# Kernel optimization log

Measured on AMD Instinct MI355X. Metric: run time of the kernel, lower is better.

Reference implementation:

```python
import jax, jax.numpy as jnp
import numpy as np

D_MODEL = 1024
N_HEADS = 16
HEAD_DIM = D_MODEL // N_HEADS  # 64
WINDOW = 128
LOCAL_BLOCK = 256
LATENT_TOKENS = 64
LATENT_D = 256
LATENT_HEADS = 4
LATENT_HD = LATENT_D // LATENT_HEADS  # 64
NEG = -1e9


def setup_inputs() -> dict:
    key = jax.random.key(0)
    ks = jax.random.split(key, 14)
    B, S = 2, 4096
    s = 0.02
    f32 = jnp.float32
    return {
        "x": jax.random.normal(ks[0], (B, S, D_MODEL), f32),
        "qkv_w": jax.random.normal(ks[1], (D_MODEL, 3 * D_MODEL), f32) * s,
        "qkv_b": jnp.zeros((3 * D_MODEL,), f32),
        "rq_w": jax.random.normal(ks[2], (D_MODEL, LATENT_D), f32) * s,
        "rq_b": jnp.zeros((LATENT_D,), f32),
        "rkv_w": jax.random.normal(ks[3], (D_MODEL, 2 * LATENT_D), f32) * s,
        "rkv_b": jnp.zeros((2 * LATENT_D,), f32),
        "rout_w": jax.random.normal(ks[4], (LATENT_D, D_MODEL), f32) * s,
        "rout_b": jnp.zeros((D_MODEL,), f32),
        "out_w": jax.random.normal(ks[5], (D_MODEL, D_MODEL), f32) * s,
        "out_b": jnp.zeros((D_MODEL,), f32),
        "gl_w": jax.random.normal(ks[6], (HEAD_DIM, 1), f32) * s,
        "gr_w": jax.random.normal(ks[7], (HEAD_DIM, 1), f32) * s,
    }


def _local_attention(q, k, v):
    # q,k,v: [B,H,S,hd]. Blockwise causal local attention: query i attends to
    # keys at distance d with 0 < d <= WINDOW (strictly past, self excluded).
    B, H, S, hd = q.shape
    bs = min(S, max(WINDOW, LOCAL_BLOCK))
    nb = S // bs  # S chosen divisible by bs
    w = WINDOW
    L = bs + w - 1  # key span per query block
    k_pad = jnp.pad(k, ((0, 0), (0, 0), (w - 1, 0), (0, 0)))
    v_pad = jnp.pad(v, ((0, 0), (0, 0), (w - 1, 0), (0, 0)))
    starts = jnp.arange(nb) * bs
    idx = starts[:, None] + jnp.arange(L)[None, :]  # [nb,L] into padded axis
    kb = k_pad[:, :, idx]  # [B,H,nb,L,hd]
    vb = v_pad[:, :, idx]
    qb = q.reshape(B, H, nb, bs, hd)
    q_pos = starts[:, None] + jnp.arange(bs)[None, :]            # [nb,bs]
    k_gpos = starts[:, None] + jnp.arange(L)[None, :] - (w - 1)   # [nb,L]
    dist = q_pos[:, :, None] - k_gpos[:, None, :]                 # [nb,bs,L]
    allowed = (dist > 0) & (dist <= w) & (k_gpos[:, None, :] >= 0)
    scale = 1.0 / np.sqrt(hd)
    scores = jnp.einsum('bhnqd,bhnkd->bhnqk', qb, kb) * scale
    scores = jnp.where(allowed, scores, NEG)
    attn = jax.nn.softmax(scores, axis=-1)
    # query 0 has no valid keys (self excluded) -> output 0 for that row
    attn = jnp.where(allowed.any(-1)[None, None, :, :, None], attn, 0.0)
    out = jnp.einsum('bhnqk,bhnkd->bhnqd', attn, vb)
    return out.reshape(B, H, S, hd)


def reference(x, qkv_w, qkv_b, rq_w, rq_b, rkv_w, rkv_b, rout_w, rout_b,
              out_w, out_b, gl_w, gr_w):
    B, S, D = x.shape
    # ---- local branch ----
    qkv = x @ qkv_w + qkv_b  # [B,S,3D]
    q, k, v = jnp.split(qkv, 3, axis=-1)
    def heads(t):
        return t.reshape(B, S, N_HEADS, HEAD_DIM).transpose(0, 2, 1, 3)
    local = _local_attention(heads(q), heads(k), heads(v))  # [B,H,S,hd]
    # ---- pooled latents ----
    chunk = -(-S // min(LATENT_TOKENS, S))  # ceil; S divisible here
    nlat = S // chunk
    pooled = x.reshape(B, nlat, chunk, D).mean(axis=2)  # [B,L,D]
    chunk_ids = jnp.arange(S) // chunk                   # [S]
    # ---- latent cross-attention ----
    rq = (x @ rq_w + rq_b).reshape(B, S, LATENT_HEADS, LATENT_HD).transpose(0, 2, 1, 3)
    rkv = pooled @ rkv_w + rkv_b
    rk, rv = jnp.split(rkv, 2, axis=-1)
    rk = rk.reshape(B, nlat, LATENT_HEADS, LATENT_HD).transpose(0, 2, 1, 3)
    rv = rv.reshape(B, nlat, LATENT_HEADS, LATENT_HD).transpose(0, 2, 1, 3)
    lscale = 1.0 / np.sqrt(LATENT_HD)
    lscores = jnp.einsum('bhsd,bhld->bhsl', rq, rk) * lscale  # [B,Hl,S,L]
    lat_allowed = jnp.arange(nlat)[None, :] < chunk_ids[:, None]  # strictly past chunks
    lscores = jnp.where(lat_allowed[None, None], lscores, NEG)
    lattn = jax.nn.softmax(lscores, axis=-1)
    lattn = jnp.where(lat_allowed.any(-1)[None, None, :, None], lattn, 0.0)
    lat_out = jnp.einsum('bhsl,bhld->bhsd', lattn, rv)  # [B,Hl,S,hdl]
    lat_out = lat_out.transpose(0, 2, 1, 3).reshape(B, S, LATENT_D)
    remote = (lat_out @ rout_w + rout_b)                 # [B,S,D]
    remote_h = remote.reshape(B, S, N_HEADS, HEAD_DIM).transpose(0, 2, 1, 3)
    # ---- learned per-head gate mixing local/remote ----
    gate = jax.nn.sigmoid(local @ gl_w + remote_h @ gr_w)  # [B,H,S,1]
    mixed = gate * local + (1.0 - gate) * remote_h
    mixed = mixed.transpose(0, 2, 1, 3).reshape(B, S, D)
    return mixed @ out_w + out_b
```

## Files before the change

kernel.cpp:

```cpp
#include <hip/hip_runtime.h>

typedef __bf16 bf16;
typedef bf16 bf16x4 __attribute__((ext_vector_type(4)));
typedef bf16 bf16x8 __attribute__((ext_vector_type(8)));
typedef float f32x4 __attribute__((ext_vector_type(4)));

#define B_ 2
#define S_ 4096
#define D_ 1024
#define QSTR 3328

__device__ __forceinline__ void gload_lds16(const void* g, void* l) {
  __builtin_amdgcn_global_load_lds((const __attribute__((address_space(1))) void*)g,
                                   (__attribute__((address_space(3))) void*)l, 16, 0, 0);
}

__device__ __forceinline__ void transpose_block(
    const float* __restrict__ in, bf16* __restrict__ out, int K, int N,
    int bx, int by, float (*tile)[33], int tx, int ty)
{
  const int nb = bx * 32, kb = by * 32;
#pragma unroll
  for (int j = 0; j < 4; j++)
    tile[ty + j * 8][tx] = in[(size_t)(kb + ty + j * 8) * N + nb + tx];
  __syncthreads();
#pragma unroll
  for (int j = 0; j < 4; j++)
    out[(size_t)(nb + ty + j * 8) * K + kb + tx] = (bf16)tile[tx][ty + j * 8];
}

__global__ __launch_bounds__(256) void prep_kernel(
    const float* __restrict__ qkv_w, const float* __restrict__ rq_w,
    const float* __restrict__ rkv_w, const float* __restrict__ rout_w,
    const float* __restrict__ out_w, const float* __restrict__ x,
    const float* __restrict__ qkv_b, const float* __restrict__ rq_b,
    bf16* __restrict__ qkvr_wt, bf16* __restrict__ rkv_wt,
    bf16* __restrict__ rout_wt, bf16* __restrict__ out_wt,
    bf16* __restrict__ xb, float* __restrict__ qkvr_b)
{
  __shared__ float tile[32][33];
  const int t = threadIdx.x;
  const int tx = t & 31, ty = t >> 5;
  int bid = blockIdx.x;
  if (bid < 3072) {
    transpose_block(qkv_w, qkvr_wt, 1024, 3072, bid % 96, bid / 96, tile, tx, ty);
    return;
  }
  bid -= 3072;
  if (bid < 256) {
    transpose_block(rq_w, qkvr_wt + (size_t)3072 * 1024, 1024, 256, bid % 8, bid / 8, tile, tx, ty);
    return;
  }
  bid -= 256;
  if (bid < 512) {
    transpose_block(rkv_w, rkv_wt, 1024, 512, bid % 16, bid / 16, tile, tx, ty);
    return;
  }
  bid -= 512;
  if (bid < 256) {
    transpose_block(rout_w, rout_wt, 256, 1024, bid % 32, bid / 32, tile, tx, ty);
    return;
  }
  bid -= 256;
  if (bid < 1024) {
    transpose_block(out_w, out_wt, 1024, 1024, bid % 32, bid / 32, tile, tx, ty);
    return;
  }
  bid -= 1024;
  if (bid < 2048) {
    const int n4 = B_ * S_ * 1024 / 4;
    for (int i = bid * 256 + t; i < n4; i += 2048 * 256) {
      const float4 v = ((const float4*)x)[i];
      bf16x4 o = {(bf16)v.x, (bf16)v.y, (bf16)v.z, (bf16)v.w};
      *(bf16x4*)&xb[i * 4] = o;
    }
    return;
  }
  {
    for (int i = t; i < 3072; i += 256) qkvr_b[i] = qkv_b[i];
    if (t < 256) qkvr_b[3072 + t] = rq_b[t];
  }
}

template <typename OutT>
__global__ __launch_bounds__(256) void gemm_bias_kernel(
    const bf16* __restrict__ A, const bf16* __restrict__ Bt,
    const float* __restrict__ bias, OutT* __restrict__ C,
    int M, int N, int K)
{
  __shared__ __align__(16) bf16 Al[128 * 32];
  __shared__ __align__(16) bf16 Bl[128 * 32];
  const int m0 = blockIdx.x * 128;
  const int n0 = blockIdx.y * 128;
  const int t = threadIdx.x;
  const int lane = t & 63;
  const int wave = t >> 6;
  const int wr = (wave >> 1) * 64;
  const int wc = (wave & 1) * 64;
  const int r16 = lane & 15;
  const int kg = lane >> 4;

  f32x4 acc[4][4];
#pragma unroll
  for (int i = 0; i < 4; i++)
#pragma unroll
    for (int j = 0; j < 4; j++) {
      f32x4 z = {0.f, 0.f, 0.f, 0.f};
      acc[i][j] = z;
    }

  for (int k0 = 0; k0 < K; k0 += 32) {
    __syncthreads();
#pragma unroll
    for (int i = 0; i < 2; i++) {
      const int o = i * 4096 + wave * 1024 + lane * 16;
      const int r = o >> 6;
      const int cb = o & 63;
      gload_lds16((const char*)(A + (size_t)(m0 + r) * K + k0) + cb,
                  (char*)Al + i * 4096 + wave * 1024);
      gload_lds16((const char*)(Bt + (size_t)(n0 + r) * K + k0) + cb,
                  (char*)Bl + i * 4096 + wave * 1024);
    }
    __syncthreads();
    bf16x8 a[4], b[4];
#pragma unroll
    for (int i = 0; i < 4; i++)
      a[i] = *(const bf16x8*)&Al[(wr + i * 16 + r16) * 32 + kg * 8];
#pragma unroll
    for (int i = 0; i < 4; i++)
      b[i] = *(const bf16x8*)&Bl[(wc + i * 16 + r16) * 32 + kg * 8];
#pragma unroll
    for (int i = 0; i < 4; i++)
#pragma unroll
      for (int j = 0; j < 4; j++)
        acc[i][j] = __builtin_amdgcn_mfma_f32_16x16x32_bf16(a[i], b[j], acc[i][j], 0, 0, 0);
  }

  float bs[4];
#pragma unroll
  for (int j = 0; j < 4; j++) bs[j] = bias[n0 + wc + j * 16 + r16];
#pragma unroll
  for (int i = 0; i < 4; i++)
#pragma unroll
    for (int j = 0; j < 4; j++)
#pragma unroll
      for (int r = 0; r < 4; r++) {
        const int row = m0 + wr + i * 16 + kg * 4 + r;
        const int col = n0 + wc + j * 16 + r16;
        C[(size_t)row * N + col] = (OutT)(acc[i][j][r] + bs[j]);
      }
}

template <typename OutT>
__global__ __launch_bounds__(512, 1) void gemm8_kernel(
    const bf16* __restrict__ A, const bf16* __restrict__ Bt,
    const float* __restrict__ bias, OutT* __restrict__ C,
    int M, int N, int K)
{
  __shared__ __align__(16) bf16 Al[2][256 * 64];
  __shared__ __align__(16) bf16 Bl[2][256 * 64];

  const int nbx = gridDim.x;
  const int nwg = nbx * gridDim.y;
  int bid = blockIdx.y * nbx + blockIdx.x;
  bid = (bid & 7) * (nwg >> 3) + (bid >> 3);
  const int m0 = (bid % nbx) * 256;
  const int n0 = (bid / nbx) * 256;

  const int t = threadIdx.x;
  const int lane = t & 63;
  const int w = t >> 6;
  const int wm = w >> 2;
  const int wn = w & 3;
  const int l15 = lane & 15;
  const int kg = lane >> 4;

  const int srow = t >> 3;
  const int schunk = (t & 7) ^ (srow & 7);
  const bf16* Aaddr = A + (size_t)(m0 + srow) * K + schunk * 8;
  const bf16* Baddr = Bt + (size_t)(n0 + srow) * K + schunk * 8;

  const int NT = K >> 6;
  const int NITER = NT >> 1;

  const int arow = wm * 128 + l15;
  const int brow = wn * 64 + l15;
  const int c0 = (kg ^ (l15 & 7)) * 16;
  const int c1 = ((4 + kg) ^ (l15 & 7)) * 16;

  f32x4 acc[8][4];
#pragma unroll
  for (int i = 0; i < 8; i++)
#pragma unroll
    for (int j = 0; j < 4; j++) { f32x4 z = {0, 0, 0, 0}; acc[i][j] = z; }

#define STG_A(buf, q, kt) gload_lds16(Aaddr + (size_t)(q) * 64 * K + (kt) * 64, \
                                      (char*)&Al[buf][0] + (q) * 8192 + w * 1024)
#define STG_B(buf, q, kt) gload_lds16(Baddr + (size_t)(q) * 64 * K + (kt) * 64, \
                                      (char*)&Bl[buf][0] + (q) * 8192 + w * 1024)
#define RD_A(buf, aq) \
  _Pragma("unroll") for (int ii = 0; ii < 4; ii++) { \
    const char* p_ = (const char*)&Al[buf][0] + (size_t)(arow + (aq) * 64 + ii * 16) * 128; \
    af[ii][0] = *(const bf16x8*)(p_ + c0); \
    af[ii][1] = *(const bf16x8*)(p_ + c1); }
#define RD_B(buf) \
  _Pragma("unroll") for (int jj = 0; jj < 4; jj++) { \
    const char* p_ = (const char*)&Bl[buf][0] + (size_t)(brow + jj * 16) * 128; \
    bfr[jj][0] = *(const bf16x8*)(p_ + c0); \
    bfr[jj][1] = *(const bf16x8*)(p_ + c1); }
#define MM(iofs, j0) \
  _Pragma("unroll") for (int ii = 0; ii < 4; ii++) \
  _Pragma("unroll") for (int jj = (j0); jj < (j0) + 2; jj++) { \
    acc[(iofs) + ii][jj] = __builtin_amdgcn_mfma_f32_16x16x32_bf16(af[ii][0], bfr[jj][0], acc[(iofs) + ii][jj], 0, 0, 0); \
    acc[(iofs) + ii][jj] = __builtin_amdgcn_mfma_f32_16x16x32_bf16(af[ii][1], bfr[jj][1], acc[(iofs) + ii][jj], 0, 0, 0); }
#define BARX __builtin_amdgcn_s_barrier()
#define LGKM0 do { asm volatile("s_waitcnt lgkmcnt(0)" ::: "memory"); \
                   __builtin_amdgcn_sched_barrier(0); } while (0)
#define PRI1 __builtin_amdgcn_s_setprio(1)
#define PRI0 __builtin_amdgcn_s_setprio(0)

#pragma unroll
  for (int q = 0; q < 4; q++) { STG_B(0, q, 0); }
#pragma unroll
  for (int q = 0; q < 4; q++) { STG_A(0, q, 0); }
#pragma unroll
  for (int q = 0; q < 4; q++) { STG_B(1, q, 1); }
#pragma unroll
  for (int q = 0; q < 4; q++) { STG_A(1, q, 1); }
  asm volatile("s_waitcnt vmcnt(8)" ::: "memory");
  BARX;

  bf16x8 af[4][2], bfr[4][2];

  for (int it = 0; it < NITER; it++) {
    const int kt0 = 2 * it;
    const bool st = (it + 1) < NITER;

    RD_A(0, 0); RD_B(0);
    BARX; LGKM0; PRI1; MM(0, 0); PRI0; BARX;
    if (st) { STG_B(0, 0, kt0 + 2); STG_B(0, 1, kt0 + 2); }
    PRI1; MM(0, 2); PRI0; BARX;
    RD_A(0, 1);
    if (st) { STG_B(0, 2, kt0 + 2); STG_B(0, 3, kt0 + 2); }
    BARX; LGKM0; PRI1; MM(4, 0); PRI0; BARX;
    if (st) { STG_A(0, 0, kt0 + 2); STG_A(0, 2, kt0 + 2); }
    PRI1; MM(4, 2); PRI0;
    asm volatile("s_waitcnt vmcnt(6)" ::: "memory");
    BARX;

    RD_A(1, 0); RD_B(1);
    if (st) { STG_A(0, 1, kt0 + 2); STG_A(0, 3, kt0 + 2); }
    BARX; LGKM0; PRI1; MM(0, 0); PRI0; BARX;
    if (st) { STG_B(1, 0, kt0 + 3); STG_B(1, 1, kt0 + 3); }
    PRI1; MM(0, 2); PRI0; BARX;
    RD_A(1, 1);
    if (st) { STG_B(1, 2, kt0 + 3); STG_B(1, 3, kt0 + 3); }
    BARX; LGKM0; PRI1; MM(4, 0); PRI0; BARX;
    if (st) { STG_A(1, 0, kt0 + 3); STG_A(1, 1, kt0 + 3);
              STG_A(1, 2, kt0 + 3); STG_A(1, 3, kt0 + 3); }
    PRI1; MM(4, 2); PRI0;
    asm volatile("s_waitcnt vmcnt(8)" ::: "memory");
    BARX;
  }

#undef STG_A
#undef STG_B
#undef RD_A
#undef RD_B
#undef MM
#undef BARX
#undef LGKM0
#undef PRI1
#undef PRI0

  float bs[4];
#pragma unroll
  for (int j = 0; j < 4; j++) bs[j] = bias[n0 + wn * 64 + j * 16 + l15];
#pragma unroll
  for (int i = 0; i < 8; i++)
#pragma unroll
    for (int j = 0; j < 4; j++)
#pragma unroll
      for (int rr = 0; rr < 4; rr++) {
        const int row = m0 + wm * 128 + i * 16 + kg * 4 + rr;
        const int col = n0 + wn * 64 + j * 16 + l15;
        C[(size_t)row * N + col] = (OutT)(acc[i][j][rr] + bs[j]);
      }
}

__global__ __launch_bounds__(256) void pool_rkv_kernel(
    const bf16* __restrict__ xb, const bf16* __restrict__ rkv_wt,
    const float* __restrict__ rkv_b, bf16* __restrict__ rkvb)
{
  __shared__ float prow[1024];
  const int blk = blockIdx.x;
  const int b = blk >> 6, lt = blk & 63;
  const int t = threadIdx.x;

  const bf16* px = xb + ((size_t)b * S_ + lt * 64) * 1024 + t * 4;
  float s0 = 0.f, s1 = 0.f, s2 = 0.f, s3 = 0.f;
#pragma unroll
  for (int c = 0; c < 64; c++) {
    bf16x4 v = *(const bf16x4*)(px + (size_t)c * 1024);
    s0 += (float)v[0]; s1 += (float)v[1]; s2 += (float)v[2]; s3 += (float)v[3];
  }
  prow[t * 4 + 0] = s0 * 0.015625f;
  prow[t * 4 + 1] = s1 * 0.015625f;
  prow[t * 4 + 2] = s2 * 0.015625f;
  prow[t * 4 + 3] = s3 * 0.015625f;
  __syncthreads();

  const int n = blockIdx.y * 256 + t;
  const bf16* wcol = rkv_wt + (size_t)n * 1024;
  float s = rkv_b[n];
#pragma unroll 4
  for (int k = 0; k < 1024; k += 8) {
    bf16x8 wv = *(const bf16x8*)(wcol + k);
#pragma unroll
    for (int j = 0; j < 8; j++) s += prow[k + j] * (float)wv[j];
  }
  rkvb[(size_t)blk * 512 + n] = (bf16)s;
}

__global__ __launch_bounds__(256) void latent_attn_kernel(
    const bf16* __restrict__ qkvrb, const bf16* __restrict__ rkvb,
    bf16* __restrict__ latout)
{
  __shared__ float rq_s[256];
  __shared__ float attn_s[4][64];
  const int blk = blockIdx.x;
  const int b = blk >> 12, s = blk & 4095;
  const int t = threadIdx.x;
  const int h = t >> 6, l = t & 63;
  const int cid = s >> 6;
  rq_s[t] = (float)qkvrb[((size_t)b * S_ + s) * QSTR + 3072 + t];
  __syncthreads();
  float val = -1e30f;
  if (l < cid) {
    const bf16* kr = rkvb + (size_t)(b * 64 + l) * 512 + h * 64;
    float sum = 0.f;
#pragma unroll
    for (int c = 0; c < 8; c++) {
      bf16x8 kv = *(const bf16x8*)(kr + c * 8);
#pragma unroll
      for (int j = 0; j < 8; j++) sum += rq_s[h * 64 + c * 8 + j] * (float)kv[j];
    }
    val = sum * 0.125f;
  }
  float mx = val;
#pragma unroll
  for (int off = 32; off; off >>= 1) mx = fmaxf(mx, __shfl_xor(mx, off));
  const float p = (l < cid) ? __expf(val - mx) : 0.f;
  float sm = p;
#pragma unroll
  for (int off = 32; off; off >>= 1) sm += __shfl_xor(sm, off);
  attn_s[h][l] = (sm > 0.f) ? p / sm : 0.f;
  __syncthreads();
  float o = 0.f;
  const bf16* vb = rkvb + (size_t)b * 64 * 512 + 256 + h * 64 + l;
  for (int lat = 0; lat < cid; lat++) o += attn_s[h][lat] * (float)vb[(size_t)lat * 512];
  latout[((size_t)b * S_ + s) * 256 + h * 64 + l] = (bf16)o;
}

__global__ __launch_bounds__(256) void local_attn_gate(
    const bf16* __restrict__ qkv, const bf16* __restrict__ remote,
    const float* __restrict__ glw, const float* __restrict__ grw,
    bf16* __restrict__ mixedb)
{
  __shared__ __align__(16) bf16 Kl[128 * 72];
  __shared__ __align__(16) bf16 Vt[64 * 136];

  const int q0 = blockIdx.x * 128;
  const int h  = blockIdx.y;
  const int b  = blockIdx.z;
  const int t  = threadIdx.x;
  const int w  = t >> 6;
  const int l  = t & 63;
  const int g  = l >> 4;
  const int l15 = l & 15;

  const bf16* qbase = qkv + (size_t)b * S_ * QSTR + h * 64;
  const bf16* kbase = qbase + 1024;
  const bf16* vbase = qbase + 2048;

  bf16* PlW = &Kl[w * 32 * 72];

  const int kq = (t & 31) * 4;
  const int dh = (t >> 5) * 8;

  bf16x8 qf[2][2];
#pragma unroll
  for (int qg = 0; qg < 2; qg++)
#pragma unroll
    for (int db = 0; db < 2; db++)
      qf[qg][db] = *(const bf16x8*)(qbase + (size_t)(q0 + w * 32 + qg * 16 + l15) * QSTR + db * 32 + g * 8);

  float m_[2][4], l_[2][4];
  f32x4 accO[2][4];
#pragma unroll
  for (int qg = 0; qg < 2; qg++) {
#pragma unroll
    for (int r = 0; r < 4; r++) { m_[qg][r] = -1e30f; l_[qg][r] = 0.f; }
#pragma unroll
    for (int dt = 0; dt < 4; dt++) { f32x4 z = {0,0,0,0}; accO[qg][dt] = z; }
  }

  const int tstart = (q0 == 0) ? 1 : 0;

  bf16x8 kreg[4], vreg[4];
  {
    const int base = q0 - 128 + tstart * 128;
#pragma unroll
    for (int i = 0; i < 4; i++) {
      const int c = i * 256 + t;
      const int kk = c >> 3, dc = c & 7;
      kreg[i] = *(const bf16x8*)(kbase + (size_t)(base + kk) * QSTR + dc * 8);
    }
#pragma unroll
    for (int i = 0; i < 4; i++)
      vreg[i] = *(const bf16x8*)(vbase + (size_t)(base + kq + i) * QSTR + dh);
  }

  for (int tile = tstart; tile < 2; tile++) {
    __syncthreads();
#pragma unroll
    for (int i = 0; i < 4; i++) {
      const int c = i * 256 + t;
      const int kk = c >> 3, dc = c & 7;
      *(bf16x8*)&Kl[kk * 72 + dc * 8] = kreg[i];
    }
#pragma unroll
    for (int j = 0; j < 8; j++) {
      bf16x4 wv = {vreg[0][j], vreg[1][j], vreg[2][j], vreg[3][j]};
      *(bf16x4*)&Vt[(dh + j) * 136 + kq] = wv;
    }
    __syncthreads();
    if (tile == 0) {
#pragma unroll
      for (int i = 0; i < 4; i++) {
        const int c = i * 256 + t;
        const int kk = c >> 3, dc = c & 7;
        kreg[i] = *(const bf16x8*)(kbase + (size_t)(q0 + kk) * QSTR + dc * 8);
      }
#pragma unroll
      for (int i = 0; i < 4; i++)
        vreg[i] = *(const bf16x8*)(vbase + (size_t)(q0 + kq + i) * QSTR + dh);
    }

    const int kt_lo = (tile == 0) ? 2 * w : 0;
    const int kt_hi = (tile == 0) ? 8 : 2 * w + 2;
    const int nkt = kt_hi - kt_lo;

    f32x4 s[2][8];
#pragma unroll
    for (int qg = 0; qg < 2; qg++)
#pragma unroll
      for (int kk = 0; kk < 8; kk++) { f32x4 z = {0,0,0,0}; s[qg][kk] = z; }

#pragma unroll
    for (int kk = 0; kk < 8; kk++) {
      if (kk >= nkt) continue;
      const int kt = kt_lo + kk;
      const bf16x8 kf0 = *(const bf16x8*)&Kl[(kt * 16 + l15) * 72 + g * 8];
      const bf16x8 kf1 = *(const bf16x8*)&Kl[(kt * 16 + l15) * 72 + 32 + g * 8];
      s[0][kk] = __builtin_amdgcn_mfma_f32_16x16x32_bf16(qf[0][0], kf0, s[0][kk], 0, 0, 0);
      s[0][kk] = __builtin_amdgcn_mfma_f32_16x16x32_bf16(qf[0][1], kf1, s[0][kk], 0, 0, 0);
      s[1][kk] = __builtin_amdgcn_mfma_f32_16x16x32_bf16(qf[1][0], kf0, s[1][kk], 0, 0, 0);
      s[1][kk] = __builtin_amdgcn_mfma_f32_16x16x32_bf16(qf[1][1], kf1, s[1][kk], 0, 0, 0);
    }
    asm volatile("s_waitcnt lgkmcnt(0)" ::: "memory");
    __builtin_amdgcn_s_barrier();

#pragma unroll
    for (int qg = 0; qg < 2; qg++) {
#pragma unroll
      for (int kk = 0; kk < 8; kk++) {
        if (kk >= nkt) continue;
        const int kr = (kt_lo + kk) * 16 + l15;
#pragma unroll
        for (int r = 0; r < 4; r++) {
          const int qr = w * 32 + qg * 16 + g * 4 + r;
          const bool ok = (tile == 0) ? (kr >= qr) : (kr < qr);
          s[qg][kk][r] = ok ? s[qg][kk][r] * 0.125f : -1e9f;
        }
      }
      float corr[4];
#pragma unroll
      for (int r = 0; r < 4; r++) {
        float v = -1e30f;
#pragma unroll
        for (int kk = 0; kk < 8; kk++) { if (kk >= nkt) continue; v = fmaxf(v, s[qg][kk][r]); }
        v = fmaxf(v, __shfl_xor(v, 1));
        v = fmaxf(v, __shfl_xor(v, 2));
        v = fmaxf(v, __shfl_xor(v, 4));
        v = fmaxf(v, __shfl_xor(v, 8));
        const float mn = fmaxf(m_[qg][r], v);
        corr[r] = __expf(m_[qg][r] - mn);
        m_[qg][r] = mn;
      }
      float rs[4] = {0.f, 0.f, 0.f, 0.f};
#pragma unroll
      for (int kk = 0; kk < 8; kk++) {
        if (kk >= nkt) continue;
        const int kt = kt_lo + kk;
#pragma unroll
        for (int r = 0; r < 4; r++) {
          const float sv = s[qg][kk][r];
          const float p = (sv > -5e8f) ? __expf(sv - m_[qg][r]) : 0.f;
          rs[r] += p;
          PlW[(g * 4 + r) * 136 + kt * 16 + l15] = (bf16)p;
        }
      }
#pragma unroll
      for (int r = 0; r < 4; r++) {
        float v = rs[r];
        v += __shfl_xor(v, 1); v += __shfl_xor(v, 2);
        v += __shfl_xor(v, 4); v += __shfl_xor(v, 8);
        l_[qg][r] = l_[qg][r] * corr[r] + v;
#pragma unroll
        for (int dt = 0; dt < 4; dt++) accO[qg][dt][r] *= corr[r];
      }
      asm volatile("s_waitcnt lgkmcnt(0)" ::: "memory");
      __builtin_amdgcn_sched_barrier(0);
      const int kc_lo = (tile == 0) ? w : 0;
      const int kc_hi = (tile == 0) ? 4 : w + 1;
#pragma unroll
      for (int kc = 0; kc < 4; kc++) {
        if (kc < kc_lo || kc >= kc_hi) continue;
        const bf16x8 pa = *(const bf16x8*)&PlW[l15 * 136 + kc * 32 + g * 8];
#pragma unroll
        for (int dt = 0; dt < 4; dt++) {
          const bf16x8 vf = *(const bf16x8*)&Vt[(dt * 16 + l15) * 136 + kc * 32 + g * 8];
          accO[qg][dt] = __builtin_amdgcn_mfma_f32_16x16x32_bf16(pa, vf, accO[qg][dt], 0, 0, 0);
        }
      }
    }
  }

  float glv[4], grv[4];
#pragma unroll
  for (int dt = 0; dt < 4; dt++) {
    glv[dt] = glw[dt * 16 + l15];
    grv[dt] = grw[dt * 16 + l15];
  }
  bf16* outp = mixedb + ((size_t)b * S_ + q0 + w * 32) * 1024 + h * 64;
  const bf16* rbase = remote + ((size_t)b * S_ + q0 + w * 32) * 1024 + h * 64;
#pragma unroll
  for (int qg = 0; qg < 2; qg++)
#pragma unroll
    for (int r = 0; r < 4; r++) {
      const int row = qg * 16 + g * 4 + r;
      const float inv = (l_[qg][r] > 0.f) ? 1.f / l_[qg][r] : 0.f;
      float lv[4], rv[4];
      float part = 0.f;
#pragma unroll
      for (int dt = 0; dt < 4; dt++) {
        lv[dt] = accO[qg][dt][r] * inv;
        rv[dt] = (float)rbase[(size_t)row * 1024 + dt * 16 + l15];
        part += lv[dt] * glv[dt] + rv[dt] * grv[dt];
      }
      part += __shfl_xor(part, 1);
      part += __shfl_xor(part, 2);
      part += __shfl_xor(part, 4);
      part += __shfl_xor(part, 8);
      const float gg = 1.f / (1.f + __expf(-part));
#pragma unroll
      for (int dt = 0; dt < 4; dt++)
        outp[(size_t)row * 1024 + dt * 16 + l15] = (bf16)(gg * lv[dt] + (1.f - gg) * rv[dt]);
    }
}

extern "C" void kernel_launch(void* const* d_in, const int* in_sizes, int n_in,
                              void* d_out, int out_size, void* d_ws, size_t ws_size,
                              hipStream_t stream)
{
  const float* x      = (const float*)d_in[0];
  const float* qkv_w  = (const float*)d_in[1];
  const float* qkv_b  = (const float*)d_in[2];
  const float* rq_w   = (const float*)d_in[3];
  const float* rq_b   = (const float*)d_in[4];
  const float* rkv_w  = (const float*)d_in[5];
  const float* rkv_b  = (const float*)d_in[6];
  const float* rout_w = (const float*)d_in[7];
  const float* rout_b = (const float*)d_in[8];
  const float* out_w  = (const float*)d_in[9];
  const float* out_b  = (const float*)d_in[10];
  const float* gl_w   = (const float*)d_in[11];
  const float* gr_w   = (const float*)d_in[12];

  char* w = (char*)d_ws;
  bf16* qkvr_wt = (bf16*)w; w += (size_t)QSTR * 1024 * 2;
  bf16* rkv_wt  = (bf16*)w; w += (size_t)512 * 1024 * 2;
  bf16* rout_wt = (bf16*)w; w += (size_t)1024 * 256 * 2;
  bf16* out_wt  = (bf16*)w; w += (size_t)1024 * 1024 * 2;
  float* qkvr_b = (float*)w; w += (size_t)QSTR * 4;
  bf16* xb      = (bf16*)w; w += (size_t)B_ * S_ * 1024 * 2;
  bf16* qkvrb   = (bf16*)w; w += (size_t)B_ * S_ * QSTR * 2;
  bf16* rkvb    = (bf16*)w; w += (size_t)B_ * 64 * 512 * 2;
  bf16* latout  = (bf16*)w; w += (size_t)B_ * S_ * 256 * 2;
  bf16* remote  = (bf16*)w; w += (size_t)B_ * S_ * 1024 * 2;
  bf16* mixedb  = (bf16*)w; w += (size_t)B_ * S_ * 1024 * 2;

  prep_kernel<<<dim3(7169), 256, 0, stream>>>(qkv_w, rq_w, rkv_w, rout_w, out_w, x,
                                              qkv_b, rq_b,
                                              qkvr_wt, rkv_wt, rout_wt, out_wt, xb, qkvr_b);

  gemm8_kernel<bf16><<<dim3(32, 13), 512, 0, stream>>>(xb, qkvr_wt, qkvr_b, qkvrb, B_ * S_, QSTR, 1024);
  pool_rkv_kernel<<<dim3(128, 2), 256, 0, stream>>>(xb, rkv_wt, rkv_b, rkvb);
  latent_attn_kernel<<<dim3(B_ * S_), 256, 0, stream>>>(qkvrb, rkvb, latout);
  gemm_bias_kernel<bf16><<<dim3(64, 8), 256, 0, stream>>>(latout, rout_wt, rout_b, remote, B_ * S_, 1024, 256);
  local_attn_gate<<<dim3(S_ / 128, 16, B_), 256, 0, stream>>>(qkvrb, remote, gl_w, gr_w, mixedb);
  gemm_bias_kernel<float><<<dim3(64, 8), 256, 0, stream>>>(mixedb, out_wt, out_b, (float*)d_out, B_ * S_, 1024, 1024);
}
```

Baseline: 252.3 us.

## Balance causal local-attention work across waves with paired query slices

Each wave now takes two 16-row query slices, j=w and j=7-w, instead of two adjacent slices. The triangular causal mask gives different slices very different key-tile counts, so pairing one short slice with one long slice evens the MFMA work across the four waves. P is staged in a dedicated LDS buffer rather than aliased onto the K tile. That removes the barrier between QK and softmax, and each slice runs QK, softmax and PV in sequence. The cost is extra LDS (about 17KB more), which may lower occupancy, and less MFMA interleaving between the two slices.

```diff
diff --git a/kernel.cpp b/kernel.cpp
--- a/kernel.cpp
+++ b/kernel.cpp
@@ -369,6 +369,7 @@
 {
   __shared__ __align__(16) bf16 Kl[128 * 72];
   __shared__ __align__(16) bf16 Vt[64 * 136];
+  __shared__ __align__(16) bf16 Pl[4][16 * 136];
 
   const int q0 = blockIdx.x * 128;
   const int h  = blockIdx.y;
@@ -383,26 +384,28 @@
   const bf16* kbase = qbase + 1024;
   const bf16* vbase = qbase + 2048;
 
-  bf16* PlW = &Kl[w * 32 * 72];
+  bf16* PlW = &Pl[w][0];
 
   const int kq = (t & 31) * 4;
   const int dh = (t >> 5) * 8;
 
   bf16x8 qf[2][2];
 #pragma unroll
-  for (int qg = 0; qg < 2; qg++)
+  for (int sl = 0; sl < 2; sl++) {
+    const int j = sl ? 7 - w : w;
 #pragma unroll
     for (int db = 0; db < 2; db++)
-      qf[qg][db] = *(const bf16x8*)(qbase + (size_t)(q0 + w * 32 + qg * 16 + l15) * QSTR + db * 32 + g * 8);
+      qf[sl][db] = *(const bf16x8*)(qbase + (size_t)(q0 + j * 16 + l15) * QSTR + db * 32 + g * 8);
+  }
 
   float m_[2][4], l_[2][4];
   f32x4 accO[2][4];
 #pragma unroll
-  for (int qg = 0; qg < 2; qg++) {
-#pragma unroll
-    for (int r = 0; r < 4; r++) { m_[qg][r] = -1e30f; l_[qg][r] = 0.f; }
-#pragma unroll
-    for (int dt = 0; dt < 4; dt++) { f32x4 z = {0,0,0,0}; accO[qg][dt] = z; }
+  for (int sl = 0; sl < 2; sl++) {
+#pragma unroll
+    for (int r = 0; r < 4; r++) { m_[sl][r] = -1e30f; l_[sl][r] = 0.f; }
+#pragma unroll
+    for (int dt = 0; dt < 4; dt++) { f32x4 z = {0,0,0,0}; accO[sl][dt] = z; }
   }
 
   const int tstart = (q0 == 0) ? 1 : 0;
@@ -447,41 +450,32 @@
         vreg[i] = *(const bf16x8*)(vbase + (size_t)(q0 + kq + i) * QSTR + dh);
     }
 
-    const int kt_lo = (tile == 0) ? 2 * w : 0;
-    const int kt_hi = (tile == 0) ? 8 : 2 * w + 2;
-    const int nkt = kt_hi - kt_lo;
-
-    f32x4 s[2][8];
-#pragma unroll
-    for (int qg = 0; qg < 2; qg++)
-#pragma unroll
-      for (int kk = 0; kk < 8; kk++) { f32x4 z = {0,0,0,0}; s[qg][kk] = z; }
-
-#pragma unroll
-    for (int kk = 0; kk < 8; kk++) {
-      if (kk >= nkt) continue;
-      const int kt = kt_lo + kk;
-      const bf16x8 kf0 = *(const bf16x8*)&Kl[(kt * 16 + l15) * 72 + g * 8];
-      const bf16x8 kf1 = *(const bf16x8*)&Kl[(kt * 16 + l15) * 72 + 32 + g * 8];
-      s[0][kk] = __builtin_amdgcn_mfma_f32_16x16x32_bf16(qf[0][0], kf0, s[0][kk], 0, 0, 0);
-      s[0][kk] = __builtin_amdgcn_mfma_f32_16x16x32_bf16(qf[0][1], kf1, s[0][kk], 0, 0, 0);
-      s[1][kk] = __builtin_amdgcn_mfma_f32_16x16x32_bf16(qf[1][0], kf0, s[1][kk], 0, 0, 0);
-      s[1][kk] = __builtin_amdgcn_mfma_f32_16x16x32_bf16(qf[1][1], kf1, s[1][kk], 0, 0, 0);
-    }
-    asm volatile("s_waitcnt lgkmcnt(0)" ::: "memory");
-    __builtin_amdgcn_s_barrier();
-
-#pragma unroll
-    for (int qg = 0; qg < 2; qg++) {
+#pragma unroll
+    for (int sl = 0; sl < 2; sl++) {
+      const int j = sl ? 7 - w : w;
+      const int lo = (tile == 0) ? (j & ~1) : 0;
+      const int hi = (tile == 0) ? 8 : ((j & ~1) + 2);
+
+      f32x4 s[8];
 #pragma unroll
       for (int kk = 0; kk < 8; kk++) {
-        if (kk >= nkt) continue;
-        const int kr = (kt_lo + kk) * 16 + l15;
+        if (kk < lo || kk >= hi) continue;
+        f32x4 z = {0,0,0,0};
+        s[kk] = z;
+        const bf16x8 kf0 = *(const bf16x8*)&Kl[(kk * 16 + l15) * 72 + g * 8];
+        const bf16x8 kf1 = *(const bf16x8*)&Kl[(kk * 16 + l15) * 72 + 32 + g * 8];
+        s[kk] = __builtin_amdgcn_mfma_f32_16x16x32_bf16(qf[sl][0], kf0, s[kk], 0, 0, 0);
+        s[kk] = __builtin_amdgcn_mfma_f32_16x16x32_bf16(qf[sl][1], kf1, s[kk], 0, 0, 0);
+      }
+#pragma unroll
+      for (int kk = 0; kk < 8; kk++) {
+        if (kk < lo || kk >= hi) continue;
+        const int kr = kk * 16 + l15;
 #pragma unroll
         for (int r = 0; r < 4; r++) {
-          const int qr = w * 32 + qg * 16 + g * 4 + r;
+          const int qr = j * 16 + g * 4 + r;
           const bool ok = (tile == 0) ? (kr >= qr) : (kr < qr);
-          s[qg][kk][r] = ok ? s[qg][kk][r] * 0.125f : -1e9f;
+          s[kk][r] = ok ? s[kk][r] * 0.125f : -1e9f;
         }
       }
       float corr[4];
@@ -489,26 +483,25 @@
       for (int r = 0; r < 4; r++) {
         float v = -1e30f;
 #pragma unroll
-        for (int kk = 0; kk < 8; kk++) { if (kk >= nkt) continue; v = fmaxf(v, s[qg][kk][r]); }
+        for (int kk = 0; kk < 8; kk++) { if (kk < lo || kk >= hi) continue; v = fmaxf(v, s[kk][r]); }
         v = fmaxf(v, __shfl_xor(v, 1));
         v = fmaxf(v, __shfl_xor(v, 2));
         v = fmaxf(v, __shfl_xor(v, 4));
         v = fmaxf(v, __shfl_xor(v, 8));
-        const float mn = fmaxf(m_[qg][r], v);
-        corr[r] = __expf(m_[qg][r] - mn);
-        m_[qg][r] = mn;
+        const float mn = fmaxf(m_[sl][r], v);
+        corr[r] = __expf(m_[sl][r] - mn);
+        m_[sl][r] = mn;
       }
       float rs[4] = {0.f, 0.f, 0.f, 0.f};
 #pragma unroll
       for (int kk = 0; kk < 8; kk++) {
-        if (kk >= nkt) continue;
-        const int kt = kt_lo + kk;
+        if (kk < lo || kk >= hi) continue;
 #pragma unroll
         for (int r = 0; r < 4; r++) {
-          const float sv = s[qg][kk][r];
-          const float p = (sv > -5e8f) ? __expf(sv - m_[qg][r]) : 0.f;
+          const float sv = s[kk][r];
+          const float p = (sv > -5e8f) ? __expf(sv - m_[sl][r]) : 0.f;
           rs[r] += p;
-          PlW[(g * 4 + r) * 136 + kt * 16 + l15] = (bf16)p;
+          PlW[(g * 4 + r) * 136 + kk * 16 + l15] = (bf16)p;
         }
       }
 #pragma unroll
@@ -516,22 +509,22 @@
         float v = rs[r];
         v += __shfl_xor(v, 1); v += __shfl_xor(v, 2);
         v += __shfl_xor(v, 4); v += __shfl_xor(v, 8);
-        l_[qg][r] = l_[qg][r] * corr[r] + v;
-#pragma unroll
-        for (int dt = 0; dt < 4; dt++) accO[qg][dt][r] *= corr[r];
+        l_[sl][r] = l_[sl][r] * corr[r] + v;
+#pragma unroll
+        for (int dt = 0; dt < 4; dt++) accO[sl][dt][r] *= corr[r];
       }
       asm volatile("s_waitcnt lgkmcnt(0)" ::: "memory");
       __builtin_amdgcn_sched_barrier(0);
-      const int kc_lo = (tile == 0) ? w : 0;
-      const int kc_hi = (tile == 0) ? 4 : w + 1;
+      const int clo = (tile == 0) ? (j >> 1) : 0;
+      const int chi = (tile == 0) ? 4 : ((j >> 1) + 1);
 #pragma unroll
       for (int kc = 0; kc < 4; kc++) {
-        if (kc < kc_lo || kc >= kc_hi) continue;
+        if (kc < clo || kc >= chi) continue;
         const bf16x8 pa = *(const bf16x8*)&PlW[l15 * 136 + kc * 32 + g * 8];
 #pragma unroll
         for (int dt = 0; dt < 4; dt++) {
           const bf16x8 vf = *(const bf16x8*)&Vt[(dt * 16 + l15) * 136 + kc * 32 + g * 8];
-          accO[qg][dt] = __builtin_amdgcn_mfma_f32_16x16x32_bf16(pa, vf, accO[qg][dt], 0, 0, 0);
+          accO[sl][dt] = __builtin_amdgcn_mfma_f32_16x16x32_bf16(pa, vf, accO[sl][dt], 0, 0, 0);
         }
       }
     }
@@ -543,19 +536,20 @@
     glv[dt] = glw[dt * 16 + l15];
     grv[dt] = grw[dt * 16 + l15];
   }
-  bf16* outp = mixedb + ((size_t)b * S_ + q0 + w * 32) * 1024 + h * 64;
-  const bf16* rbase = remote + ((size_t)b * S_ + q0 + w * 32) * 1024 + h * 64;
-#pragma unroll
-  for (int qg = 0; qg < 2; qg++)
+  bf16* outp = mixedb + ((size_t)b * S_ + q0) * 1024 + h * 64;
+  const bf16* rbase = remote + ((size_t)b * S_ + q0) * 1024 + h * 64;
+#pragma unroll
+  for (int sl = 0; sl < 2; sl++) {
+    const int j = sl ? 7 - w : w;
 #pragma unroll
     for (int r = 0; r < 4; r++) {
-      const int row = qg * 16 + g * 4 + r;
-      const float inv = (l_[qg][r] > 0.f) ? 1.f / l_[qg][r] : 0.f;
+      const int row = j * 16 + g * 4 + r;
+      const float inv = (l_[sl][r] > 0.f) ? 1.f / l_[sl][r] : 0.f;
       float lv[4], rv[4];
       float part = 0.f;
 #pragma unroll
       for (int dt = 0; dt < 4; dt++) {
-        lv[dt] = accO[qg][dt][r] * inv;
+        lv[dt] = accO[sl][dt][r] * inv;
         rv[dt] = (float)rbase[(size_t)row * 1024 + dt * 16 + l15];
         part += lv[dt] * glv[dt] + rv[dt] * grv[dt];
       }
@@ -568,6 +562,7 @@
       for (int dt = 0; dt < 4; dt++)
         outp[(size_t)row * 1024 + dt * 16 + l15] = (bf16)(gg * lv[dt] + (1.f - gg) * rv[dt]);
     }
+  }
 }
 
 extern "C" void kernel_launch(void* const* d_in, const int* in_sizes, int n_in,
```

Measured after the change: 240.7 us. 1.05x faster.
